# Optimization experiments

Hardware: AMD Instinct MI355X
Metric: run time of the kernel (lower is better)

Reference implementation:

```python
import jax, jax.numpy as jnp
import numpy as np

DIM = 1024
HEADS = 16
HEAD_DIM = DIM // HEADS
SCALE = HEAD_DIM ** -0.5


def setup_inputs() -> dict:
    key = jax.random.key(0)
    ks = jax.random.split(key, 6)
    B, N = 2, 2048
    s = DIM ** -0.5
    return {
        "x": jax.random.normal(ks[0], (B, N, DIM), dtype=jnp.float32),
        "Wq": jax.random.normal(ks[1], (DIM, DIM), dtype=jnp.float32) * s,
        "Wk": jax.random.normal(ks[2], (DIM, DIM), dtype=jnp.float32) * s,
        "Wv": jax.random.normal(ks[3], (DIM, DIM), dtype=jnp.float32) * s,
        "Wo": jax.random.normal(ks[4], (DIM, DIM), dtype=jnp.float32) * s,
        "bo": jnp.zeros((DIM,), dtype=jnp.float32),
    }


def reference(x, Wq, Wk, Wv, Wo, bo):
    B, N, D = x.shape
    # Linear projections (torch Linear: y = x @ W.T)
    q = x @ Wq.T
    k = x @ Wk.T
    v = x @ Wv.T
    # [B, H, N, hd]
    q = q.reshape(B, N, HEADS, HEAD_DIM).transpose(0, 2, 1, 3)
    k = k.reshape(B, N, HEADS, HEAD_DIM).transpose(0, 2, 1, 3)
    v = v.reshape(B, N, HEADS, HEAD_DIM).transpose(0, 2, 1, 3)
    scores = jnp.einsum('bhid,bhjd->bhij', q, k) * SCALE
    probs = jax.nn.softmax(scores, axis=-1)
    out = jnp.einsum('bhij,bhjd->bhid', probs, v)
    out = out.transpose(0, 2, 1, 3).reshape(B, N, D)
    return out @ Wo.T + bo
```

## Files before the change

kernel.cpp:

```cpp
#include <hip/hip_runtime.h>

#define DIM    1024
#define HEADS  16
#define HD     64
#define BATCH  2
#define SEQ    2048
#define C2     0.18033688011112042f

typedef __attribute__((ext_vector_type(8))) short           short8;
typedef __attribute__((ext_vector_type(4))) short           short4v;
typedef __attribute__((ext_vector_type(4))) float           f4;
typedef __attribute__((ext_vector_type(4))) unsigned short  u16x4;
typedef __attribute__((ext_vector_type(4))) unsigned int    u32x4;
typedef __attribute__((ext_vector_type(2))) unsigned int    u32x2;

typedef __attribute__((address_space(3))) unsigned int       as3_u32;
typedef const __attribute__((address_space(1))) unsigned int as1_u32;

__device__ __forceinline__ unsigned short f2bf(float f) {
    unsigned int u = __builtin_bit_cast(unsigned int, f);
    u = (u + 0x7fffu + ((u >> 16) & 1u)) >> 16;
    return (unsigned short)u;
}
__device__ __forceinline__ unsigned int pk_bf16(float a, float b) {
    return (unsigned int)f2bf(a) | ((unsigned int)f2bf(b) << 16);
}
__device__ __forceinline__ unsigned int pk_bf16_hw(float a, float b) {
    unsigned int r;
    asm("v_cvt_pk_bf16_f32 %0, %1, %2" : "=v"(r) : "v"(a), "v"(b));
    return r;
}

#if __has_builtin(__builtin_amdgcn_exp2f)
#define EXP2(x) __builtin_amdgcn_exp2f(x)
#else
#define EXP2(x) exp2f(x)
#endif

__device__ __forceinline__ void gl2lds16(const unsigned short* g, unsigned short* l) {
    __builtin_amdgcn_global_load_lds((as1_u32*)g, (as3_u32*)l, 16, 0, 0);
}

__global__ __launch_bounds__(256) void k_cast_all(
    const float* __restrict__ x,  const float* __restrict__ wq,
    const float* __restrict__ wk, const float* __restrict__ wv,
    const float* __restrict__ wo, unsigned short* __restrict__ dst)
{
    const int i = blockIdx.x * 256 + threadIdx.x;
    const float* src;
    int off;
    if (i < (1 << 20))            { src = x;  off = 0; }
    else if (i < (5 << 18))       { src = wq; off = 1 << 20; }
    else if (i < (6 << 18))       { src = wk; off = 5 << 18; }
    else if (i < (7 << 18))       { src = wv; off = 6 << 18; }
    else                          { src = wo; off = 7 << 18; }
    f4 v = ((const f4*)src)[i - off];
    u16x4 o;
    o[0] = f2bf(v[0]); o[1] = f2bf(v[1]); o[2] = f2bf(v[2]); o[3] = f2bf(v[3]);
    ((u16x4*)dst)[i] = o;
}

__global__ __launch_bounds__(256) void gemm_qkv(
    const unsigned short* __restrict__ A,
    const unsigned short* __restrict__ Wq,
    const unsigned short* __restrict__ Wk,
    const unsigned short* __restrict__ Wv,
    unsigned short* __restrict__ Qo,
    unsigned short* __restrict__ Ko,
    unsigned short* __restrict__ Vo)
{
    __shared__ __align__(16) unsigned short Xs[128 * 64];
    __shared__ __align__(16) unsigned short Ws[128 * 64];
    const int L   = blockIdx.x;
    const int xcd = L & 7;
    const int idx = L >> 3;
    const int col = idx >> 2;
    const int sb  = (xcd * 4 + (idx & 3)) * 128;
    const int wsel = col >> 3;
    const int fb   = (col & 7) * 128;
    const unsigned short* W = (wsel == 0) ? Wq : ((wsel == 1) ? Wk : Wv);

    const int tid  = threadIdx.x;
    const int wave = tid >> 6, lane = tid & 63;
    const int quad = lane >> 4, l16 = lane & 15;
    const int wm = (wave & 1) << 6, wn = (wave >> 1) << 6;

    const unsigned short* aLDS = (wsel < 2) ? Ws : Xs;
    const unsigned short* bLDS = (wsel < 2) ? Xs : Ws;

    f4 acc[4][4] = {};

    for (int k0 = 0; k0 < DIM; k0 += 64) {
        __syncthreads();
        #pragma unroll
        for (int i = 0; i < 4; i++) {
            const int c = tid + (i << 8);
            const int row = c >> 3;
            const int cb  = (c & 7) ^ (row & 7);
            gl2lds16(&A[(size_t)(sb + row) * DIM + k0 + (cb << 3)],
                     &Xs[(size_t)((i << 8) + (wave << 6)) * 8]);
            gl2lds16(&W[(size_t)(fb + row) * DIM + k0 + (cb << 3)],
                     &Ws[(size_t)((i << 8) + (wave << 6)) * 8]);
        }
        __syncthreads();
        #pragma unroll
        for (int ks = 0; ks < 2; ks++) {
            short8 afr[4], bfr[4];
            #pragma unroll
            for (int i = 0; i < 4; i++) {
                const int row = wm + i * 16 + l16;
                afr[i] = *(const short8*)(&aLDS[row * 64 + (((ks * 4 + quad) ^ (row & 7)) << 3)]);
            }
            #pragma unroll
            for (int j = 0; j < 4; j++) {
                const int row = wn + j * 16 + l16;
                bfr[j] = *(const short8*)(&bLDS[row * 64 + (((ks * 4 + quad) ^ (row & 7)) << 3)]);
            }
            #pragma unroll
            for (int i = 0; i < 4; i++)
                #pragma unroll
                for (int j = 0; j < 4; j++)
                    acc[i][j] = __builtin_amdgcn_mfma_f32_16x16x32_bf16(afr[i], bfr[j], acc[i][j], 0, 0, 0);
        }
    }

    if (wsel < 2) {
        unsigned short* out = (wsel == 0) ? Qo : Ko;
        const float sc = (wsel == 0) ? C2 : 1.0f;
        #pragma unroll
        for (int j = 0; j < 4; j++) {
            const int ms = sb + wn + j * 16 + l16;
            const int b = ms >> 11, ns = ms & (SEQ - 1);
            #pragma unroll
            for (int i = 0; i < 4; i++) {
                const int feat = fb + wm + i * 16 + quad * 4;
                const int h = feat >> 6, d = feat & (HD - 1);
                u32x2 pw;
                pw[0] = pk_bf16(acc[i][j][0] * sc, acc[i][j][1] * sc);
                pw[1] = pk_bf16(acc[i][j][2] * sc, acc[i][j][3] * sc);
                *(u32x2*)(&out[((size_t)(b * HEADS + h) * SEQ + ns) * HD + d]) = pw;
            }
        }
    } else {
        #pragma unroll
        for (int j = 0; j < 4; j++) {
            const int feat = fb + wn + j * 16 + l16;
            const int h = feat >> 6, d = feat & (HD - 1);
            #pragma unroll
            for (int i = 0; i < 4; i++) {
                const int ms = sb + wm + i * 16 + quad * 4;
                const int b = ms >> 11, ns = ms & (SEQ - 1);
                u32x2 pw;
                pw[0] = pk_bf16(acc[i][j][0], acc[i][j][1]);
                pw[1] = pk_bf16(acc[i][j][2], acc[i][j][3]);
                *(u32x2*)(&Vo[((size_t)(b * HEADS + h) * HD + d) * SEQ + ns]) = pw;
            }
        }
    }
}

__global__ __launch_bounds__(256, 2) void attn_fwd(
    const unsigned short* __restrict__ Qg,
    const unsigned short* __restrict__ Kg,
    const unsigned short* __restrict__ VTg,
    unsigned short* __restrict__ AOb)
{
    __shared__ __align__(16) unsigned short Ks [2][64 * 72];
    __shared__ __align__(16) unsigned short VsT[2][64 * 72];
#if !__has_builtin(__builtin_amdgcn_mfma_f32_16x16x16bf16_1k)
    __shared__ __align__(16) unsigned short Ps[128 * 72];
#endif

    const int L   = blockIdx.x;
    const int xcd = L & 7;
    const int idx = L >> 3;
    const int bh  = xcd * 4 + (idx >> 4);
    const int q0  = (idx & 15) << 7;

    const unsigned short* Qb  = Qg  + (size_t)bh * SEQ * HD;
    const unsigned short* Kb  = Kg  + (size_t)bh * SEQ * HD;
    const unsigned short* VTb = VTg + (size_t)bh * HD * SEQ;

    const int tid  = threadIdx.x;
    const int wave = tid >> 6, lane = tid & 63;
    const int quad = lane >> 4, l16 = lane & 15;
    const int qw   = wave << 5;
    const int r8   = tid >> 3;
    const int g8   = (tid & 7) * 8;

    short8 qf[2][2];
    #pragma unroll
    for (int nf = 0; nf < 2; nf++)
        #pragma unroll
        for (int ks = 0; ks < 2; ks++)
            qf[nf][ks] = *(const short8*)(&Qb[(size_t)(q0 + qw + nf * 16 + l16) * HD + ks * 32 + quad * 8]);

    #pragma unroll
    for (int p = 0; p < 2; p++) {
        const int row = r8 + p * 32;
        *(u32x4*)(&Ks [0][row * 72 + g8]) = *(const u32x4*)(&Kb [(size_t)row * HD + g8]);
        *(u32x4*)(&VsT[0][row * 72 + g8]) = *(const u32x4*)(&VTb[(size_t)row * SEQ + g8]);
    }
    __syncthreads();

    f4 lsum[2] = {};
    f4 Oacc[4][2] = {};
    int cur = 0;

    for (int kt = 0; kt < SEQ / 64; kt++) {
        u32x4 kpre[2], vpre[2];
        if (kt < SEQ / 64 - 1) {
            #pragma unroll
            for (int p = 0; p < 2; p++) {
                const int row = r8 + p * 32;
                kpre[p] = *(const u32x4*)(&Kb [(size_t)((kt + 1) * 64 + row) * HD + g8]);
                vpre[p] = *(const u32x4*)(&VTb[(size_t)row * SEQ + (kt + 1) * 64 + g8]);
            }
        }
        const unsigned short* ksb = &Ks [cur][0];
        const unsigned short* vsb = &VsT[cur][0];

        f4 sacc[4][2] = {};
        __builtin_amdgcn_s_setprio(1);
        #pragma unroll
        for (int ks = 0; ks < 2; ks++) {
            short8 kfr[4];
            #pragma unroll
            for (int mf = 0; mf < 4; mf++)
                kfr[mf] = *(const short8*)(&ksb[(mf * 16 + l16) * 72 + ks * 32 + quad * 8]);
            #pragma unroll
            for (int mf = 0; mf < 4; mf++)
                #pragma unroll
                for (int nf = 0; nf < 2; nf++)
                    sacc[mf][nf] = __builtin_amdgcn_mfma_f32_16x16x32_bf16(kfr[mf], qf[nf][ks], sacc[mf][nf], 0, 0, 0);
        }
        __builtin_amdgcn_s_setprio(0);

#if __has_builtin(__builtin_amdgcn_mfma_f32_16x16x16bf16_1k)
        #pragma unroll
        for (int mf = 0; mf < 4; mf++) {
            short4v vfr[4];
            #pragma unroll
            for (int d = 0; d < 4; d++)
                vfr[d] = *(const short4v*)(&vsb[(d * 16 + l16) * 72 + mf * 16 + quad * 4]);
            short4v pbx[2];
            #pragma unroll
            for (int nf = 0; nf < 2; nf++) {
                f4 pv;
                #pragma unroll
                for (int r = 0; r < 4; r++)
                    pv[r] = EXP2(sacc[mf][nf][r]);
                lsum[nf] += pv;
                u32x2 pw;
                pw[0] = pk_bf16_hw(pv[0], pv[1]);
                pw[1] = pk_bf16_hw(pv[2], pv[3]);
                pbx[nf] = __builtin_bit_cast(short4v, pw);
            }
            #pragma unroll
            for (int d = 0; d < 4; d++)
                #pragma unroll
                for (int nf = 0; nf < 2; nf++)
                    Oacc[d][nf] = __builtin_amdgcn_mfma_f32_16x16x16bf16_1k(vfr[d], pbx[nf], Oacc[d][nf], 0, 0, 0);
        }
#else
        #pragma unroll
        for (int nf = 0; nf < 2; nf++) {
            #pragma unroll
            for (int mf = 0; mf < 4; mf++) {
                f4 pv;
                #pragma unroll
                for (int r = 0; r < 4; r++)
                    pv[r] = EXP2(sacc[mf][nf][r]);
                lsum[nf] += pv;
                u32x2 pw;
                pw[0] = pk_bf16(pv[0], pv[1]);
                pw[1] = pk_bf16(pv[2], pv[3]);
                *(u32x2*)(&Ps[(qw + nf * 16 + l16) * 72 + mf * 16 + quad * 4]) = pw;
            }
        }
        #pragma unroll
        for (int ks = 0; ks < 2; ks++) {
            short8 vfr[4], pf[2];
            #pragma unroll
            for (int mf = 0; mf < 4; mf++)
                vfr[mf] = *(const short8*)(&vsb[(mf * 16 + l16) * 72 + ks * 32 + quad * 8]);
            #pragma unroll
            for (int nf = 0; nf < 2; nf++)
                pf[nf] = *(const short8*)(&Ps[(qw + nf * 16 + l16) * 72 + ks * 32 + quad * 8]);
            #pragma unroll
            for (int mf = 0; mf < 4; mf++)
                #pragma unroll
                for (int nf = 0; nf < 2; nf++)
                    Oacc[mf][nf] = __builtin_amdgcn_mfma_f32_16x16x32_bf16(vfr[mf], pf[nf], Oacc[mf][nf], 0, 0, 0);
        }
#endif

        if (kt < SEQ / 64 - 1) {
            #pragma unroll
            for (int p = 0; p < 2; p++) {
                const int row = r8 + p * 32;
                *(u32x4*)(&Ks [cur ^ 1][row * 72 + g8]) = kpre[p];
                *(u32x4*)(&VsT[cur ^ 1][row * 72 + g8]) = vpre[p];
            }
            __syncthreads();
        }
        cur ^= 1;
    }

    const int b = bh >> 4, h = bh & (HEADS - 1);
    #pragma unroll
    for (int nf = 0; nf < 2; nf++) {
        float l = lsum[nf][0] + lsum[nf][1] + lsum[nf][2] + lsum[nf][3];
        l += __shfl_xor(l, 16);
        l += __shfl_xor(l, 32);
        const float inv = 1.0f / l;
        const int qg = q0 + qw + nf * 16 + l16;
        #pragma unroll
        for (int mf = 0; mf < 4; mf++) {
            u32x2 o;
            o[0] = pk_bf16_hw(Oacc[mf][nf][0] * inv, Oacc[mf][nf][1] * inv);
            o[1] = pk_bf16_hw(Oacc[mf][nf][2] * inv, Oacc[mf][nf][3] * inv);
            *(u32x2*)(&AOb[(size_t)(b * SEQ + qg) * DIM + h * HD + mf * 16 + quad * 4]) = o;
        }
    }
}

__global__ __launch_bounds__(256) void gemm_out(
    const unsigned short* __restrict__ AO,
    const unsigned short* __restrict__ W,
    float* __restrict__ out,
    const float* __restrict__ bias)
{
    __shared__ __align__(16) unsigned short As[64 * 64];
    __shared__ __align__(16) unsigned short Bs[128 * 64];
    const int L   = blockIdx.x;
    const int xcd = L & 7;
    const int idx = L >> 3;
    const int n0  = (xcd * 4 + (idx >> 4)) * 128;
    const int m0  = (idx & 15) * 64;

    const int tid  = threadIdx.x;
    const int wave = tid >> 6, lane = tid & 63;
    const int quad = lane >> 4, l16 = lane & 15;
    const int wm = (wave & 1) << 5, wn = (wave >> 1) << 6;

    f4 acc[2][4] = {};

    for (int k0 = 0; k0 < DIM; k0 += 64) {
        __syncthreads();
        #pragma unroll
        for (int i = 0; i < 2; i++) {
            const int c = tid + (i << 8);
            const int row = c >> 3;
            const int cb  = (c & 7) ^ (row & 7);
            gl2lds16(&W[(size_t)(m0 + row) * DIM + k0 + (cb << 3)],
                     &As[(size_t)((i << 8) + (wave << 6)) * 8]);
        }
        #pragma unroll
        for (int i = 0; i < 4; i++) {
            const int c = tid + (i << 8);
            const int row = c >> 3;
            const int cb  = (c & 7) ^ (row & 7);
            gl2lds16(&AO[(size_t)(n0 + row) * DIM + k0 + (cb << 3)],
                     &Bs[(size_t)((i << 8) + (wave << 6)) * 8]);
        }
        __syncthreads();
        #pragma unroll
        for (int ks = 0; ks < 2; ks++) {
            short8 afr[2], bfr[4];
            #pragma unroll
            for (int i = 0; i < 2; i++) {
                const int row = wm + i * 16 + l16;
                afr[i] = *(const short8*)(&As[row * 64 + (((ks * 4 + quad) ^ (row & 7)) << 3)]);
            }
            #pragma unroll
            for (int j = 0; j < 4; j++) {
                const int row = wn + j * 16 + l16;
                bfr[j] = *(const short8*)(&Bs[row * 64 + (((ks * 4 + quad) ^ (row & 7)) << 3)]);
            }
            #pragma unroll
            for (int i = 0; i < 2; i++)
                #pragma unroll
                for (int j = 0; j < 4; j++)
                    acc[i][j] = __builtin_amdgcn_mfma_f32_16x16x32_bf16(afr[i], bfr[j], acc[i][j], 0, 0, 0);
        }
    }

    #pragma unroll
    for (int i = 0; i < 2; i++) {
        const int feat = m0 + wm + i * 16 + quad * 4;
        const f4 bv = *(const f4*)(&bias[feat]);
        #pragma unroll
        for (int j = 0; j < 4; j++) {
            const int ns = n0 + wn + j * 16 + l16;
            *(f4*)(&out[(size_t)ns * DIM + feat]) = acc[i][j] + bv;
        }
    }
}

extern "C" void kernel_launch(void* const* d_in, const int* in_sizes, int n_in,
                              void* d_out, int out_size, void* d_ws, size_t ws_size,
                              hipStream_t stream) {
    (void)in_sizes; (void)n_in; (void)out_size; (void)ws_size;
    const float* x  = (const float*)d_in[0];
    const float* Wq = (const float*)d_in[1];
    const float* Wk = (const float*)d_in[2];
    const float* Wv = (const float*)d_in[3];
    const float* Wo = (const float*)d_in[4];
    const float* bo = (const float*)d_in[5];

    unsigned short* wsu = (unsigned short*)d_ws;
    unsigned short* xb  = wsu;
    unsigned short* Wqb = wsu + (4u  << 20);
    unsigned short* Wkb = wsu + (5u  << 20);
    unsigned short* Wvb = wsu + (6u  << 20);
    unsigned short* Wob = wsu + (7u  << 20);
    unsigned short* Qb  = wsu + (8u  << 20);
    unsigned short* Kb  = wsu + (12u << 20);
    unsigned short* VTb = wsu + (16u << 20);
    unsigned short* AOb = wsu + (20u << 20);

    k_cast_all<<<8192, 256, 0, stream>>>(x, Wq, Wk, Wv, Wo, wsu);

    gemm_qkv<<<768, 256, 0, stream>>>(xb, Wqb, Wkb, Wvb, Qb, Kb, VTb);

    attn_fwd<<<512, 256, 0, stream>>>(Qb, Kb, VTb, AOb);

    gemm_out<<<512, 256, 0, stream>>>(AOb, Wob, (float*)d_out, bo);
}
```

Baseline: 173.2 us.

## Fuse fp32-to-bf16 casts into GEMM tile loads, drop separate cast kernel

Removes the standalone cast kernel and has gemm_qkv and gemm_out read fp32 x and weights directly, convert them to bf16 in registers and store them into padded LDS tiles (stride 72). This drops one launch and the write-then-reread of the bf16 copies. In exchange, the GEMMs read twice as many bytes per tile and re-convert inputs redundantly across blocks: x is reread by 24 column blocks and each weight by many row blocks. The async global-to-LDS path is also replaced with register-staged loads, which adds latency and register pressure.

```diff
diff --git a/kernel.cpp b/kernel.cpp
--- a/kernel.cpp
+++ b/kernel.cpp
@@ -41,36 +41,17 @@
     __builtin_amdgcn_global_load_lds((as1_u32*)g, (as3_u32*)l, 16, 0, 0);
 }
 
-__global__ __launch_bounds__(256) void k_cast_all(
-    const float* __restrict__ x,  const float* __restrict__ wq,
-    const float* __restrict__ wk, const float* __restrict__ wv,
-    const float* __restrict__ wo, unsigned short* __restrict__ dst)
-{
-    const int i = blockIdx.x * 256 + threadIdx.x;
-    const float* src;
-    int off;
-    if (i < (1 << 20))            { src = x;  off = 0; }
-    else if (i < (5 << 18))       { src = wq; off = 1 << 20; }
-    else if (i < (6 << 18))       { src = wk; off = 5 << 18; }
-    else if (i < (7 << 18))       { src = wv; off = 6 << 18; }
-    else                          { src = wo; off = 7 << 18; }
-    f4 v = ((const f4*)src)[i - off];
-    u16x4 o;
-    o[0] = f2bf(v[0]); o[1] = f2bf(v[1]); o[2] = f2bf(v[2]); o[3] = f2bf(v[3]);
-    ((u16x4*)dst)[i] = o;
-}
-
 __global__ __launch_bounds__(256) void gemm_qkv(
-    const unsigned short* __restrict__ A,
-    const unsigned short* __restrict__ Wq,
-    const unsigned short* __restrict__ Wk,
-    const unsigned short* __restrict__ Wv,
+    const float* __restrict__ x,
+    const float* __restrict__ Wq,
+    const float* __restrict__ Wk,
+    const float* __restrict__ Wv,
     unsigned short* __restrict__ Qo,
     unsigned short* __restrict__ Ko,
     unsigned short* __restrict__ Vo)
 {
-    __shared__ __align__(16) unsigned short Xs[128 * 64];
-    __shared__ __align__(16) unsigned short Ws[128 * 64];
+    __shared__ __align__(16) unsigned short Xs[128 * 72];
+    __shared__ __align__(16) unsigned short Ws[128 * 72];
     const int L   = blockIdx.x;
     const int xcd = L & 7;
     const int idx = L >> 3;
@@ -78,7 +59,7 @@
     const int sb  = (xcd * 4 + (idx & 3)) * 128;
     const int wsel = col >> 3;
     const int fb   = (col & 7) * 128;
-    const unsigned short* W = (wsel == 0) ? Wq : ((wsel == 1) ? Wk : Wv);
+    const float* W = (wsel == 0) ? Wq : ((wsel == 1) ? Wk : Wv);
 
     const int tid  = threadIdx.x;
     const int wave = tid >> 6, lane = tid & 63;
@@ -92,30 +73,36 @@
 
     for (int k0 = 0; k0 < DIM; k0 += 64) {
         __syncthreads();
-        #pragma unroll
-        for (int i = 0; i < 4; i++) {
-            const int c = tid + (i << 8);
-            const int row = c >> 3;
-            const int cb  = (c & 7) ^ (row & 7);
-            gl2lds16(&A[(size_t)(sb + row) * DIM + k0 + (cb << 3)],
-                     &Xs[(size_t)((i << 8) + (wave << 6)) * 8]);
-            gl2lds16(&W[(size_t)(fb + row) * DIM + k0 + (cb << 3)],
-                     &Ws[(size_t)((i << 8) + (wave << 6)) * 8]);
+        f4 xa[8], wa[8];
+        #pragma unroll
+        for (int i = 0; i < 8; i++) {
+            const int f = (i << 8) + tid;
+            const int row = f >> 4, c4 = f & 15;
+            xa[i] = ((const f4*)(x + (size_t)(sb + row) * DIM + k0))[c4];
+            wa[i] = ((const f4*)(W + (size_t)(fb + row) * DIM + k0))[c4];
+        }
+        #pragma unroll
+        for (int i = 0; i < 8; i++) {
+            const int f = (i << 8) + tid;
+            const int row = f >> 4, c4 = f & 15;
+            u32x2 px, pw2;
+            px[0]  = pk_bf16_hw(xa[i][0], xa[i][1]);
+            px[1]  = pk_bf16_hw(xa[i][2], xa[i][3]);
+            pw2[0] = pk_bf16_hw(wa[i][0], wa[i][1]);
+            pw2[1] = pk_bf16_hw(wa[i][2], wa[i][3]);
+            *(u32x2*)(&Xs[row * 72 + c4 * 4]) = px;
+            *(u32x2*)(&Ws[row * 72 + c4 * 4]) = pw2;
         }
         __syncthreads();
         #pragma unroll
         for (int ks = 0; ks < 2; ks++) {
             short8 afr[4], bfr[4];
             #pragma unroll
-            for (int i = 0; i < 4; i++) {
-                const int row = wm + i * 16 + l16;
-                afr[i] = *(const short8*)(&aLDS[row * 64 + (((ks * 4 + quad) ^ (row & 7)) << 3)]);
-            }
-            #pragma unroll
-            for (int j = 0; j < 4; j++) {
-                const int row = wn + j * 16 + l16;
-                bfr[j] = *(const short8*)(&bLDS[row * 64 + (((ks * 4 + quad) ^ (row & 7)) << 3)]);
-            }
+            for (int i = 0; i < 4; i++)
+                afr[i] = *(const short8*)(&aLDS[(wm + i * 16 + l16) * 72 + ks * 32 + quad * 8]);
+            #pragma unroll
+            for (int j = 0; j < 4; j++)
+                bfr[j] = *(const short8*)(&bLDS[(wn + j * 16 + l16) * 72 + ks * 32 + quad * 8]);
             #pragma unroll
             for (int i = 0; i < 4; i++)
                 #pragma unroll
@@ -327,11 +314,11 @@
 
 __global__ __launch_bounds__(256) void gemm_out(
     const unsigned short* __restrict__ AO,
-    const unsigned short* __restrict__ W,
+    const float* __restrict__ W,
     float* __restrict__ out,
     const float* __restrict__ bias)
 {
-    __shared__ __align__(16) unsigned short As[64 * 64];
+    __shared__ __align__(16) unsigned short As[64 * 72];
     __shared__ __align__(16) unsigned short Bs[128 * 64];
     const int L   = blockIdx.x;
     const int xcd = L & 7;
@@ -348,13 +335,12 @@
 
     for (int k0 = 0; k0 < DIM; k0 += 64) {
         __syncthreads();
-        #pragma unroll
-        for (int i = 0; i < 2; i++) {
-            const int c = tid + (i << 8);
-            const int row = c >> 3;
-            const int cb  = (c & 7) ^ (row & 7);
-            gl2lds16(&W[(size_t)(m0 + row) * DIM + k0 + (cb << 3)],
-                     &As[(size_t)((i << 8) + (wave << 6)) * 8]);
+        f4 wv4[4];
+        #pragma unroll
+        for (int i = 0; i < 4; i++) {
+            const int f = (i << 8) + tid;
+            const int row = f >> 4, c4 = f & 15;
+            wv4[i] = ((const f4*)(W + (size_t)(m0 + row) * DIM + k0))[c4];
         }
         #pragma unroll
         for (int i = 0; i < 4; i++) {
@@ -364,15 +350,22 @@
             gl2lds16(&AO[(size_t)(n0 + row) * DIM + k0 + (cb << 3)],
                      &Bs[(size_t)((i << 8) + (wave << 6)) * 8]);
         }
+        #pragma unroll
+        for (int i = 0; i < 4; i++) {
+            const int f = (i << 8) + tid;
+            const int row = f >> 4, c4 = f & 15;
+            u32x2 pw2;
+            pw2[0] = pk_bf16_hw(wv4[i][0], wv4[i][1]);
+            pw2[1] = pk_bf16_hw(wv4[i][2], wv4[i][3]);
+            *(u32x2*)(&As[row * 72 + c4 * 4]) = pw2;
+        }
         __syncthreads();
         #pragma unroll
         for (int ks = 0; ks < 2; ks++) {
             short8 afr[2], bfr[4];
             #pragma unroll
-            for (int i = 0; i < 2; i++) {
-                const int row = wm + i * 16 + l16;
-                afr[i] = *(const short8*)(&As[row * 64 + (((ks * 4 + quad) ^ (row & 7)) << 3)]);
-            }
+            for (int i = 0; i < 2; i++)
+                afr[i] = *(const short8*)(&As[(wm + i * 16 + l16) * 72 + ks * 32 + quad * 8]);
             #pragma unroll
             for (int j = 0; j < 4; j++) {
                 const int row = wn + j * 16 + l16;
@@ -410,21 +403,14 @@
     const float* bo = (const float*)d_in[5];
 
     unsigned short* wsu = (unsigned short*)d_ws;
-    unsigned short* xb  = wsu;
-    unsigned short* Wqb = wsu + (4u  << 20);
-    unsigned short* Wkb = wsu + (5u  << 20);
-    unsigned short* Wvb = wsu + (6u  << 20);
-    unsigned short* Wob = wsu + (7u  << 20);
     unsigned short* Qb  = wsu + (8u  << 20);
     unsigned short* Kb  = wsu + (12u << 20);
     unsigned short* VTb = wsu + (16u << 20);
     unsigned short* AOb = wsu + (20u << 20);
 
-    k_cast_all<<<8192, 256, 0, stream>>>(x, Wq, Wk, Wv, Wo, wsu);
-
-    gemm_qkv<<<768, 256, 0, stream>>>(xb, Wqb, Wkb, Wvb, Qb, Kb, VTb);
+    gemm_qkv<<<768, 256, 0, stream>>>(x, Wq, Wk, Wv, Qb, Kb, VTb);
 
     attn_fwd<<<512, 256, 0, stream>>>(Qb, Kb, VTb, AOb);
 
-    gemm_out<<<512, 256, 0, stream>>>(AOb, Wob, (float*)d_out, bo);
-}
+    gemm_out<<<512, 256, 0, stream>>>(AOb, Wo, (float*)d_out, bo);
+}
```

Result: slower. 196.5 us (+13.4%).
